# Kernel optimization log

Hardware: AMD Instinct MI355X
Metric: run time of the kernel (lower is better)

## Reference

```python
import jax, jax.numpy as jnp
import numpy as np

N, B, FIN, FOUT = 4096, 16, 128, 128
DENSITY = 0.01


def setup_inputs() -> dict:
    key = jax.random.key(0)
    k1, k2, k3, k4 = jax.random.split(key, 4)
    # sparse binary adjacency (static pattern), stored dense for the reference
    adj = (jax.random.uniform(k1, (N, N)) < DENSITY).astype(jnp.float32)
    x = jax.random.normal(k2, (B, N, FIN), dtype=jnp.float32)
    W = jax.random.normal(k3, (FOUT, FIN), dtype=jnp.float32) * (1.0 / np.sqrt(FIN))
    b = jax.random.normal(k4, (FOUT,), dtype=jnp.float32) * 0.01
    return {"adj": adj, "x": x, "W": W, "b": b}


def _normalized_adj(adj):
    # A_hat = D^{-1/2} (A + I) D^{-1/2}, degrees from column sums (dim=0 in torch)
    a_self = adj + jnp.eye(adj.shape[0], dtype=adj.dtype)
    dinv = jax.lax.rsqrt(jnp.sum(a_self, axis=0))
    return dinv[:, None] * a_self * dinv[None, :]


def reference(adj, x, W, b):
    a_norm = _normalized_adj(adj)
    # SpMM aggregation over nodes: (N,N) x (B,N,F) -> (B,N,F)
    agg = jnp.einsum('nm,bmf->bnf', a_norm, x)
    # dense linear transform: fc(agg)
    return jnp.einsum('bnf,of->bno', agg, W) + b
```

## Files before the change

kernel.cpp:

```cpp
#include <hip/hip_runtime.h>


#define NN 4096
#define FD 128
#define NB 16
#define CAP 96
#define CPAD 100

typedef float     f32x2 __attribute__((ext_vector_type(2)));
typedef float     f32x4 __attribute__((ext_vector_type(4)));
typedef _Float16  f16x4 __attribute__((ext_vector_type(4)));
typedef _Float16  f16x8 __attribute__((ext_vector_type(8)));
typedef int       i32x2 __attribute__((ext_vector_type(2)));

__global__ __launch_bounds__(256) void k_init(float* __restrict__ deg) {
    deg[blockIdx.x * 256 + threadIdx.x] = 0.0f;
}

__global__ __launch_bounds__(256) void k_build(const float* __restrict__ A,
                                               float* __restrict__ deg,
                                               int* __restrict__ cnt,
                                               unsigned short* __restrict__ csr) {
    __shared__ int sCnt[256];
    const int n = blockIdx.x, t = threadIdx.x;
    const float* row = A + (size_t)n * NN + t * 16;
    float r[16];
    *(f32x4*)&r[0]  = ((const f32x4*)row)[0];
    *(f32x4*)&r[4]  = ((const f32x4*)row)[1];
    *(f32x4*)&r[8]  = ((const f32x4*)row)[2];
    *(f32x4*)&r[12] = ((const f32x4*)row)[3];

    int c = 0;
    #pragma unroll
    for (int j = 0; j < 16; ++j) c += (r[j] != 0.0f) ? 1 : 0;
    sCnt[t] = c;
    __syncthreads();
    for (int off = 1; off < 256; off <<= 1) {
        const int v = sCnt[t];
        const int u = (t >= off) ? sCnt[t - off] : 0;
        __syncthreads();
        sCnt[t] = v + u;
        __syncthreads();
    }
    int pos = sCnt[t] - c;
    #pragma unroll
    for (int j = 0; j < 16; ++j) {
        if (r[j] != 0.0f) {
            const int m = t * 16 + j;
            if (pos < CAP) csr[(size_t)n * CAP + pos] = (unsigned short)m;
            ++pos;
            atomicAdd(&deg[m], 1.0f);
        }
    }
    if (t == 255) {
        int tot = sCnt[255];
        cnt[n] = tot < CAP ? tot : CAP;
    }
}

__global__ __launch_bounds__(256) void k_dinv(const float* __restrict__ deg,
                                              float* __restrict__ dinv) {
    const int i = blockIdx.x * 256 + threadIdx.x;
    dinv[i] = rsqrtf(1.0f + deg[i]);
}

#define XR 128
#define XP 136
__global__ __launch_bounds__(256) void k_xform(const float* __restrict__ x,
                                               const float* __restrict__ W,
                                               _Float16* __restrict__ y) {
    __shared__ _Float16 sX[XR][XP];
    __shared__ _Float16 sW[FD][XP];
    const int t = threadIdx.x;
    const size_t rbase = (size_t)blockIdx.x * XR;

    #pragma unroll
    for (int i = 0; i < 8; ++i) {
        const int id = t + i * 256;
        const int o = id >> 4, f8 = (id & 15) * 8;
        const f32x4 a = *(const f32x4*)&W[(size_t)o * FD + f8];
        const f32x4 b = *(const f32x4*)&W[(size_t)o * FD + f8 + 4];
        f16x8 h;
        h[0]=(_Float16)a.x; h[1]=(_Float16)a.y; h[2]=(_Float16)a.z; h[3]=(_Float16)a.w;
        h[4]=(_Float16)b.x; h[5]=(_Float16)b.y; h[6]=(_Float16)b.z; h[7]=(_Float16)b.w;
        *(f16x8*)&sW[o][f8] = h;
    }
    #pragma unroll
    for (int i = 0; i < 8; ++i) {
        const int id = t + i * 256;
        const int r = id >> 4, f8 = (id & 15) * 8;
        const f32x4 a = *(const f32x4*)&x[(rbase + r) * FD + f8];
        const f32x4 b = *(const f32x4*)&x[(rbase + r) * FD + f8 + 4];
        f16x8 h;
        h[0]=(_Float16)a.x; h[1]=(_Float16)a.y; h[2]=(_Float16)a.z; h[3]=(_Float16)a.w;
        h[4]=(_Float16)b.x; h[5]=(_Float16)b.y; h[6]=(_Float16)b.z; h[7]=(_Float16)b.w;
        *(f16x8*)&sX[r][f8] = h;
    }
    __syncthreads();

    const int w = t >> 6, lane = t & 63;
    const int lrow = lane & 15, koct = (lane >> 4) * 8;
    f32x4 acc[2][8] = {};
    #pragma unroll
    for (int kc = 0; kc < 4; ++kc) {
        const int ko = kc * 32 + koct;
        f16x8 aa0 = *(const f16x8*)&sX[w * 32 + lrow][ko];
        f16x8 aa1 = *(const f16x8*)&sX[w * 32 + 16 + lrow][ko];
        #pragma unroll
        for (int nt = 0; nt < 8; ++nt) {
            const f16x8 bb = *(const f16x8*)&sW[nt * 16 + lrow][ko];
            acc[0][nt] = __builtin_amdgcn_mfma_f32_16x16x32_f16(aa0, bb, acc[0][nt], 0, 0, 0);
            acc[1][nt] = __builtin_amdgcn_mfma_f32_16x16x32_f16(aa1, bb, acc[1][nt], 0, 0, 0);
        }
    }
    #pragma unroll
    for (int mt = 0; mt < 2; ++mt) {
        const size_t row0 = rbase + w * 32 + mt * 16 + (lane >> 4) * 4;
        #pragma unroll
        for (int nt = 0; nt < 8; ++nt) {
            const int col = nt * 16 + (lane & 15);
            #pragma unroll
            for (int r = 0; r < 4; ++r)
                y[(row0 + r) * FD + col] = (_Float16)acc[mt][nt][r];
        }
    }
}

__global__ __launch_bounds__(256) void k_agg2(const _Float16* __restrict__ y,
                                              const int* __restrict__ cnt,
                                              const unsigned short* __restrict__ csr,
                                              const float* __restrict__ dinv,
                                              const float* __restrict__ bias,
                                              float* __restrict__ out) {
    __shared__ int sL[4][CPAD * 2];
    const int t = threadIdx.x, w = t >> 6, lane = t & 63;
    const int bid = blockIdx.x;
    const int xcd = bid & 7;
    const int j   = bid >> 3;
    const int b   = 2 * xcd + (j >> 10);
    const int ng  = j & 1023;
    const int n   = ng * 4 + w;
    const int c = cnt[n];
    const int totPad = (c + 1 + 3) & ~3;

    for (int k = lane; k < totPad; k += 64) {
        int m; float wv;
        if (k < c)       { m = csr[(size_t)n * CAP + k]; wv = dinv[m]; }
        else if (k == c) { m = n; wv = dinv[n]; }
        else             { m = n; wv = 0.0f; }
        sL[w][2 * k]     = m << 7;
        sL[w][2 * k + 1] = __float_as_int(wv);
    }
    __syncthreads();

    const int rq = lane >> 4, fo = (lane & 15) * 8;
    const _Float16* yb = y + (size_t)b * (NN * FD) + fo;

    float acc[8] = {};
    i32x2 e = *(const i32x2*)&sL[w][2 * rq];
    f16x8 p = *(const f16x8*)(yb + e.x);
    float wt = __int_as_float(e.y);
    for (int k = rq + 4; k < totPad; k += 4) {
        const i32x2 e2 = *(const i32x2*)&sL[w][2 * k];
        const f16x8 p2 = *(const f16x8*)(yb + e2.x);
        const float wt2 = __int_as_float(e2.y);
        #pragma unroll
        for (int j2 = 0; j2 < 8; ++j2) acc[j2] = fmaf(wt, (float)p[j2], acc[j2]);
        p = p2; wt = wt2;
    }
    #pragma unroll
    for (int j2 = 0; j2 < 8; ++j2) acc[j2] = fmaf(wt, (float)p[j2], acc[j2]);

    #pragma unroll
    for (int j2 = 0; j2 < 8; ++j2) {
        acc[j2] += __shfl_xor(acc[j2], 16);
        acc[j2] += __shfl_xor(acc[j2], 32);
    }

    if (lane < 32) {
        const float dn = dinv[n];
        const int h = lane >> 4;
        const int f0 = (lane & 15) * 8 + h * 4;
        const f32x4 bb = *(const f32x4*)(bias + f0);
        f32x4 o;
        o.x = acc[h * 4 + 0] * dn + bb.x;
        o.y = acc[h * 4 + 1] * dn + bb.y;
        o.z = acc[h * 4 + 2] * dn + bb.z;
        o.w = acc[h * 4 + 3] * dn + bb.w;
        f32x4* dst = (f32x4*)(out + ((size_t)b * NN + n) * FD + f0);
        __builtin_nontemporal_store(o, dst);
    }
}

extern "C" void kernel_launch(void* const* d_in, const int* in_sizes, int n_in,
                              void* d_out, int out_size, void* d_ws, size_t ws_size,
                              hipStream_t stream) {
    const float* A    = (const float*)d_in[0];
    const float* x    = (const float*)d_in[1];
    const float* W    = (const float*)d_in[2];
    const float* bias = (const float*)d_in[3];
    float* out = (float*)d_out;

    float*          deg  = (float*)d_ws;
    float*          dinv = deg + NN;
    int*            cnt  = (int*)(dinv + NN);
    unsigned short* csr  = (unsigned short*)(cnt + NN);
    _Float16*       y    = (_Float16*)((char*)d_ws + (3 * NN * 4 + (size_t)NN * CAP * 2));

    k_init <<<NN / 256, 256, 0, stream>>>(deg);
    k_build<<<NN, 256, 0, stream>>>(A, deg, cnt, csr);
    k_dinv <<<NN / 256, 256, 0, stream>>>(deg, dinv);
    k_xform<<<(NB * NN) / XR, 256, 0, stream>>>(x, W, y);
    k_agg2 <<<(NN / 4) * NB, 256, 0, stream>>>(y, cnt, csr, dinv, bias, out);
}
```

Baseline: 87.09 us.

## Fuse adjacency build with feature transform and aggregate two batches per block

Merges the CSR/degree build and the fp16 feature-transform GEMM into one kernel with block-index dispatch so the two independent phases run concurrently. The degree-zeroing kernel is replaced by a memset. The aggregation kernel now handles two batches per block, reusing the neighbor list and weights and issuing twice as many independent gathers per iteration. This halves the aggregation grid and raises register use per thread.

```diff
diff --git a/kernel.cpp b/kernel.cpp
--- a/kernel.cpp
+++ b/kernel.cpp
@@ -5,24 +5,86 @@
 #define FD 128
 #define NB 16
 #define CAP 96
-#define CPAD 100
-
-typedef float     f32x2 __attribute__((ext_vector_type(2)));
+#define CPAD 104
+#define XB 512
+
 typedef float     f32x4 __attribute__((ext_vector_type(4)));
-typedef _Float16  f16x4 __attribute__((ext_vector_type(4)));
 typedef _Float16  f16x8 __attribute__((ext_vector_type(8)));
 typedef int       i32x2 __attribute__((ext_vector_type(2)));
 
-__global__ __launch_bounds__(256) void k_init(float* __restrict__ deg) {
-    deg[blockIdx.x * 256 + threadIdx.x] = 0.0f;
-}
-
-__global__ __launch_bounds__(256) void k_build(const float* __restrict__ A,
-                                               float* __restrict__ deg,
-                                               int* __restrict__ cnt,
-                                               unsigned short* __restrict__ csr) {
-    __shared__ int sCnt[256];
-    const int n = blockIdx.x, t = threadIdx.x;
+#define XR 128
+#define XP 136
+
+__global__ __launch_bounds__(256) void k_bx(const float* __restrict__ A,
+                                            float* __restrict__ deg,
+                                            int* __restrict__ cnt,
+                                            unsigned short* __restrict__ csr,
+                                            const float* __restrict__ x,
+                                            const float* __restrict__ W,
+                                            _Float16* __restrict__ y) {
+    __shared__ __align__(16) char smem[2 * XR * XP * 2];
+    const int t = threadIdx.x;
+
+    if (blockIdx.x < XB) {
+        _Float16 (*sX)[XP] = (_Float16(*)[XP])smem;
+        _Float16 (*sW)[XP] = (_Float16(*)[XP])(smem + XR * XP * 2);
+        const size_t rbase = (size_t)blockIdx.x * XR;
+
+        #pragma unroll
+        for (int i = 0; i < 8; ++i) {
+            const int id = t + i * 256;
+            const int o = id >> 4, f8 = (id & 15) * 8;
+            const f32x4 a = *(const f32x4*)&W[(size_t)o * FD + f8];
+            const f32x4 b = *(const f32x4*)&W[(size_t)o * FD + f8 + 4];
+            f16x8 h;
+            h[0]=(_Float16)a.x; h[1]=(_Float16)a.y; h[2]=(_Float16)a.z; h[3]=(_Float16)a.w;
+            h[4]=(_Float16)b.x; h[5]=(_Float16)b.y; h[6]=(_Float16)b.z; h[7]=(_Float16)b.w;
+            *(f16x8*)&sW[o][f8] = h;
+        }
+        #pragma unroll
+        for (int i = 0; i < 8; ++i) {
+            const int id = t + i * 256;
+            const int r = id >> 4, f8 = (id & 15) * 8;
+            const f32x4 a = *(const f32x4*)&x[(rbase + r) * FD + f8];
+            const f32x4 b = *(const f32x4*)&x[(rbase + r) * FD + f8 + 4];
+            f16x8 h;
+            h[0]=(_Float16)a.x; h[1]=(_Float16)a.y; h[2]=(_Float16)a.z; h[3]=(_Float16)a.w;
+            h[4]=(_Float16)b.x; h[5]=(_Float16)b.y; h[6]=(_Float16)b.z; h[7]=(_Float16)b.w;
+            *(f16x8*)&sX[r][f8] = h;
+        }
+        __syncthreads();
+
+        const int w = t >> 6, lane = t & 63;
+        const int lrow = lane & 15, koct = (lane >> 4) * 8;
+        f32x4 acc[2][8] = {};
+        #pragma unroll
+        for (int kc = 0; kc < 4; ++kc) {
+            const int ko = kc * 32 + koct;
+            f16x8 aa0 = *(const f16x8*)&sX[w * 32 + lrow][ko];
+            f16x8 aa1 = *(const f16x8*)&sX[w * 32 + 16 + lrow][ko];
+            #pragma unroll
+            for (int nt = 0; nt < 8; ++nt) {
+                const f16x8 bb = *(const f16x8*)&sW[nt * 16 + lrow][ko];
+                acc[0][nt] = __builtin_amdgcn_mfma_f32_16x16x32_f16(aa0, bb, acc[0][nt], 0, 0, 0);
+                acc[1][nt] = __builtin_amdgcn_mfma_f32_16x16x32_f16(aa1, bb, acc[1][nt], 0, 0, 0);
+            }
+        }
+        #pragma unroll
+        for (int mt = 0; mt < 2; ++mt) {
+            const size_t row0 = rbase + w * 32 + mt * 16 + (lane >> 4) * 4;
+            #pragma unroll
+            for (int nt = 0; nt < 8; ++nt) {
+                const int col = nt * 16 + (lane & 15);
+                #pragma unroll
+                for (int r = 0; r < 4; ++r)
+                    y[(row0 + r) * FD + col] = (_Float16)acc[mt][nt][r];
+            }
+        }
+        return;
+    }
+
+    int* sCnt = (int*)smem;
+    const int n = blockIdx.x - XB;
     const float* row = A + (size_t)n * NN + t * 16;
     float r[16];
     *(f32x4*)&r[0]  = ((const f32x4*)row)[0];
@@ -62,68 +124,6 @@
                                               float* __restrict__ dinv) {
     const int i = blockIdx.x * 256 + threadIdx.x;
     dinv[i] = rsqrtf(1.0f + deg[i]);
-}
-
-#define XR 128
-#define XP 136
-__global__ __launch_bounds__(256) void k_xform(const float* __restrict__ x,
-                                               const float* __restrict__ W,
-                                               _Float16* __restrict__ y) {
-    __shared__ _Float16 sX[XR][XP];
-    __shared__ _Float16 sW[FD][XP];
-    const int t = threadIdx.x;
-    const size_t rbase = (size_t)blockIdx.x * XR;
-
-    #pragma unroll
-    for (int i = 0; i < 8; ++i) {
-        const int id = t + i * 256;
-        const int o = id >> 4, f8 = (id & 15) * 8;
-        const f32x4 a = *(const f32x4*)&W[(size_t)o * FD + f8];
-        const f32x4 b = *(const f32x4*)&W[(size_t)o * FD + f8 + 4];
-        f16x8 h;
-        h[0]=(_Float16)a.x; h[1]=(_Float16)a.y; h[2]=(_Float16)a.z; h[3]=(_Float16)a.w;
-        h[4]=(_Float16)b.x; h[5]=(_Float16)b.y; h[6]=(_Float16)b.z; h[7]=(_Float16)b.w;
-        *(f16x8*)&sW[o][f8] = h;
-    }
-    #pragma unroll
-    for (int i = 0; i < 8; ++i) {
-        const int id = t + i * 256;
-        const int r = id >> 4, f8 = (id & 15) * 8;
-        const f32x4 a = *(const f32x4*)&x[(rbase + r) * FD + f8];
-        const f32x4 b = *(const f32x4*)&x[(rbase + r) * FD + f8 + 4];
-        f16x8 h;
-        h[0]=(_Float16)a.x; h[1]=(_Float16)a.y; h[2]=(_Float16)a.z; h[3]=(_Float16)a.w;
-        h[4]=(_Float16)b.x; h[5]=(_Float16)b.y; h[6]=(_Float16)b.z; h[7]=(_Float16)b.w;
-        *(f16x8*)&sX[r][f8] = h;
-    }
-    __syncthreads();
-
-    const int w = t >> 6, lane = t & 63;
-    const int lrow = lane & 15, koct = (lane >> 4) * 8;
-    f32x4 acc[2][8] = {};
-    #pragma unroll
-    for (int kc = 0; kc < 4; ++kc) {
-        const int ko = kc * 32 + koct;
-        f16x8 aa0 = *(const f16x8*)&sX[w * 32 + lrow][ko];
-        f16x8 aa1 = *(const f16x8*)&sX[w * 32 + 16 + lrow][ko];
-        #pragma unroll
-        for (int nt = 0; nt < 8; ++nt) {
-            const f16x8 bb = *(const f16x8*)&sW[nt * 16 + lrow][ko];
-            acc[0][nt] = __builtin_amdgcn_mfma_f32_16x16x32_f16(aa0, bb, acc[0][nt], 0, 0, 0);
-            acc[1][nt] = __builtin_amdgcn_mfma_f32_16x16x32_f16(aa1, bb, acc[1][nt], 0, 0, 0);
-        }
-    }
-    #pragma unroll
-    for (int mt = 0; mt < 2; ++mt) {
-        const size_t row0 = rbase + w * 32 + mt * 16 + (lane >> 4) * 4;
-        #pragma unroll
-        for (int nt = 0; nt < 8; ++nt) {
-            const int col = nt * 16 + (lane & 15);
-            #pragma unroll
-            for (int r = 0; r < 4; ++r)
-                y[(row0 + r) * FD + col] = (_Float16)acc[mt][nt][r];
-        }
-    }
 }
 
 __global__ __launch_bounds__(256) void k_agg2(const _Float16* __restrict__ y,
@@ -136,45 +136,57 @@
     const int t = threadIdx.x, w = t >> 6, lane = t & 63;
     const int bid = blockIdx.x;
     const int xcd = bid & 7;
-    const int j   = bid >> 3;
-    const int b   = 2 * xcd + (j >> 10);
-    const int ng  = j & 1023;
-    const int n   = ng * 4 + w;
+    const int b0  = 2 * xcd;
+    const int n   = (bid >> 3) * 4 + w;
     const int c = cnt[n];
     const int totPad = (c + 1 + 3) & ~3;
 
-    for (int k = lane; k < totPad; k += 64) {
+    for (int k = lane; k < CPAD; k += 64) {
         int m; float wv;
         if (k < c)       { m = csr[(size_t)n * CAP + k]; wv = dinv[m]; }
         else if (k == c) { m = n; wv = dinv[n]; }
         else             { m = n; wv = 0.0f; }
-        sL[w][2 * k]     = m << 7;
+        sL[w][2 * k]     = m << 8;
         sL[w][2 * k + 1] = __float_as_int(wv);
     }
     __syncthreads();
 
-    const int rq = lane >> 4, fo = (lane & 15) * 8;
-    const _Float16* yb = y + (size_t)b * (NN * FD) + fo;
-
-    float acc[8] = {};
+    const int rq = lane >> 4;
+    const int fo = (lane & 15) * 16;
+    const char* yb0 = (const char*)y + (size_t)b0 * (NN * FD * 2);
+    const char* yb1 = yb0 + (size_t)(NN * FD * 2);
+
+    float acc0[8] = {}, acc1[8] = {};
     i32x2 e = *(const i32x2*)&sL[w][2 * rq];
-    f16x8 p = *(const f16x8*)(yb + e.x);
+    int voff = e.x + fo;
+    f16x8 pA = *(const f16x8*)(yb0 + (size_t)(unsigned)voff);
+    f16x8 pB = *(const f16x8*)(yb1 + (size_t)(unsigned)voff);
     float wt = __int_as_float(e.y);
     for (int k = rq + 4; k < totPad; k += 4) {
         const i32x2 e2 = *(const i32x2*)&sL[w][2 * k];
-        const f16x8 p2 = *(const f16x8*)(yb + e2.x);
+        const int v2 = e2.x + fo;
+        const f16x8 nA = *(const f16x8*)(yb0 + (size_t)(unsigned)v2);
+        const f16x8 nB = *(const f16x8*)(yb1 + (size_t)(unsigned)v2);
         const float wt2 = __int_as_float(e2.y);
         #pragma unroll
-        for (int j2 = 0; j2 < 8; ++j2) acc[j2] = fmaf(wt, (float)p[j2], acc[j2]);
-        p = p2; wt = wt2;
-    }
-    #pragma unroll
-    for (int j2 = 0; j2 < 8; ++j2) acc[j2] = fmaf(wt, (float)p[j2], acc[j2]);
-
-    #pragma unroll
-    for (int j2 = 0; j2 < 8; ++j2) {
-        acc[j2] += __shfl_xor(acc[j2], 16);
-        acc[j2] += __shfl_xor(acc[j2], 32);
+        for (int j = 0; j < 8; ++j) {
+            acc0[j] = fmaf(wt, (float)pA[j], acc0[j]);
+            acc1[j] = fmaf(wt, (float)pB[j], acc1[j]);
+        }
+        pA = nA; pB = nB; wt = wt2;
+    }
+    #pragma unroll
+    for (int j = 0; j < 8; ++j) {
+        acc0[j] = fmaf(wt, (float)pA[j], acc0[j]);
+        acc1[j] = fmaf(wt, (float)pB[j], acc1[j]);
+    }
+
+    #pragma unroll
+    for (int j = 0; j < 8; ++j) {
+        acc0[j] += __shfl_xor(acc0[j], 16);
+        acc0[j] += __shfl_xor(acc0[j], 32);
+        acc1[j] += __shfl_xor(acc1[j], 16);
+        acc1[j] += __shfl_xor(acc1[j], 32);
     }
 
     if (lane < 32) {
@@ -182,13 +194,19 @@
         const int h = lane >> 4;
         const int f0 = (lane & 15) * 8 + h * 4;
         const f32x4 bb = *(const f32x4*)(bias + f0);
-        f32x4 o;
-        o.x = acc[h * 4 + 0] * dn + bb.x;
-        o.y = acc[h * 4 + 1] * dn + bb.y;
-        o.z = acc[h * 4 + 2] * dn + bb.z;
-        o.w = acc[h * 4 + 3] * dn + bb.w;
-        f32x4* dst = (f32x4*)(out + ((size_t)b * NN + n) * FD + f0);
-        __builtin_nontemporal_store(o, dst);
+        f32x4 o0, o1;
+        o0.x = acc0[h * 4 + 0] * dn + bb.x;
+        o0.y = acc0[h * 4 + 1] * dn + bb.y;
+        o0.z = acc0[h * 4 + 2] * dn + bb.z;
+        o0.w = acc0[h * 4 + 3] * dn + bb.w;
+        o1.x = acc1[h * 4 + 0] * dn + bb.x;
+        o1.y = acc1[h * 4 + 1] * dn + bb.y;
+        o1.z = acc1[h * 4 + 2] * dn + bb.z;
+        o1.w = acc1[h * 4 + 3] * dn + bb.w;
+        f32x4* d0 = (f32x4*)(out + ((size_t)b0 * NN + n) * FD + f0);
+        f32x4* d1 = (f32x4*)(out + ((size_t)(b0 + 1) * NN + n) * FD + f0);
+        __builtin_nontemporal_store(o0, d0);
+        __builtin_nontemporal_store(o1, d1);
     }
 }
 
@@ -207,9 +225,8 @@
     unsigned short* csr  = (unsigned short*)(cnt + NN);
     _Float16*       y    = (_Float16*)((char*)d_ws + (3 * NN * 4 + (size_t)NN * CAP * 2));
 
-    k_init <<<NN / 256, 256, 0, stream>>>(deg);
-    k_build<<<NN, 256, 0, stream>>>(A, deg, cnt, csr);
-    k_dinv <<<NN / 256, 256, 0, stream>>>(deg, dinv);
-    k_xform<<<(NB * NN) / XR, 256, 0, stream>>>(x, W, y);
-    k_agg2 <<<(NN / 4) * NB, 256, 0, stream>>>(y, cnt, csr, dinv, bias, out);
-}
+    hipMemsetAsync(deg, 0, NN * sizeof(float), stream);
+    k_bx  <<<XB + NN, 256, 0, stream>>>(A, deg, cnt, csr, x, W, y);
+    k_dinv<<<NN / 256, 256, 0, stream>>>(deg, dinv);
+    k_agg2<<<(NN / 4) * (NB / 2), 256, 0, stream>>>(y, cnt, csr, dinv, bias, out);
+}
```

New measurement: 77.22 us. 11.3% less time.
